# Performance work log

Measured on AMD Instinct MI355X. Metric: run time of the kernel, lower is better.

The kernel has to match this reference:

```python
import jax, jax.numpy as jnp
import numpy as np

O, D, E, K, H, A = 1024, 1024, 16, 4, 2048, 64  # option_dim, obs_dim, num_experts, k, moe_hidden, act_dim
LOSS_COEF = 0.01


def cv_squared(x):
    # torch .var() is unbiased (ddof=1)
    eps = 1e-10
    return jnp.var(x, ddof=1) / (jnp.mean(x) ** 2 + eps)


def setup_inputs() -> dict:
    key = jax.random.key(0)
    ks = jax.random.split(key, 8)
    s = 0.02
    return {
        "obs": jax.random.normal(ks[0], (O, D), jnp.float32),
        # original inits w_gate to zeros (degenerate top-k); use small random for a meaningful baseline
        "w_gate": jax.random.normal(ks[1], (O, D, E), jnp.float32) * s,
        "w1": jax.random.normal(ks[2], (E, D, H), jnp.float32) * s,   # expert MLP layer 1
        "b1": jnp.zeros((E, H), jnp.float32),
        "w2": jax.random.normal(ks[3], (E, H, A), jnp.float32) * s,   # expert MLP layer 2
        "b2": jnp.zeros((E, A), jnp.float32),
        "last_w": jax.random.normal(ks[4], (O, D, A), jnp.float32),   # last_w_layer
        "last_b": jax.random.normal(ks[5], (O, A), jnp.float32),      # last_b_layer
    }


def reference(obs, w_gate, w1, b1, w2, b2, last_w, last_b):
    # ---- noisy_top_k_gating (this version applies no noise) ----
    logits = jnp.einsum('od,ode->oe', obs, w_gate)                    # [O, E]
    top_vals, top_idx = jax.lax.top_k(logits, K + 1)
    topk_gates = jax.nn.softmax(top_vals[:, :K], axis=1)              # softmax over top-k logits
    rows = jnp.arange(O)[:, None]
    gates = jnp.zeros_like(logits).at[rows, top_idx[:, :K]].set(topk_gates)  # scatter -> [O, E]
    importance = gates.sum(axis=1)
    load = (gates > 0).sum(axis=1).astype(jnp.float32)                # faithful to original (sum over dim 1)
    loss = (cv_squared(importance) + cv_squared(load)) * LOSS_COEF
    # ---- dispatch / expert MLPs / combine (dense-over-experts equivalent; zero gates kill non-top-k) ----
    h = jax.nn.relu(jnp.einsum('od,edh->oeh', obs, w1) + b1[None])    # [O, E, H]
    y = jnp.einsum('oe,oeh,eha->oa', gates, h, w2) + gates @ b2       # [O, A]
    # ---- action head ----
    mu = jnp.einsum('od,oda->oa', obs, last_w) + last_b               # [O, A]
    action_probs = jax.nn.softmax(mu, axis=-1)
    z = (action_probs == 0.0).astype(action_probs.dtype) * 1e-08
    log_action_probs = jnp.log(action_probs + z)
    return (action_probs, log_action_probs, y, loss)
```

## Files before the change

### kernel.cpp

```cpp
#include <hip/hip_runtime.h>
#include <hip/hip_bf16.h>
#include <math.h>

#define O_ 1024
#define D_ 1024
#define E_ 16
#define K_ 4
#define H_ 2048
#define A_ 64
#define LOSS_COEF 0.01f

#define FLT_MIN_NORMAL 1.17549435e-38f

using floatx4 = __attribute__((ext_vector_type(4))) float;
using fragb   = __attribute__((ext_vector_type(8))) short;

static __device__ __forceinline__ ushort f2bf(float f) {
    unsigned u = __builtin_bit_cast(unsigned, f);
    u += 0x7fffu + ((u >> 16) & 1u);
    return (ushort)(u >> 16);
}

static __device__ __forceinline__ void gld_lds16(const void* g, void* l) {
    __builtin_amdgcn_global_load_lds(
        (const __attribute__((address_space(1))) void*)g,
        (__attribute__((address_space(3))) void*)l, 16, 0, 0);
}

__global__ __launch_bounds__(256) void gating_kernel(
    const float* __restrict__ obs, const float* __restrict__ w_gate,
    int* __restrict__ topk_idx, float* __restrict__ topk_gate,
    float* __restrict__ imp, float* __restrict__ loadv)
{
    const int o = blockIdx.x;
    const int t = threadIdx.x;
    __shared__ float xs[D_];
    __shared__ float part[64][20];
    __shared__ float logits[E_];

    const float4* xrow = (const float4*)(obs + (size_t)o * D_);
    for (int i = t; i < D_ / 4; i += 256) ((float4*)xs)[i] = xrow[i];
    __syncthreads();

    const int dg = t >> 2, e4 = t & 3;
    const float4* wg = (const float4*)(w_gate + (size_t)o * (D_ * E_));
    float4 acc = make_float4(0.f, 0.f, 0.f, 0.f);
    #pragma unroll 4
    for (int i = 0; i < 16; ++i) {
        int d = dg + (i << 6);
        float4 w = wg[d * 4 + e4];
        float x = xs[d];
        acc.x += x * w.x; acc.y += x * w.y; acc.z += x * w.z; acc.w += x * w.w;
    }
    *(float4*)&part[dg][e4 * 4] = acc;
    __syncthreads();
    if (t < E_) {
        float s = 0.f;
        for (int g = 0; g < 64; ++g) s += part[g][t];
        logits[t] = s;
    }
    __syncthreads();
    if (t == 0) {
        float lv[E_];
        #pragma unroll
        for (int i = 0; i < E_; ++i) lv[i] = logits[i];
        int idx[K_]; float val[K_];
        bool used[E_] = {};
        for (int k = 0; k < K_; ++k) {
            int bi = 0; float bv = -INFINITY;
            for (int i = 0; i < E_; ++i)
                if (!used[i] && lv[i] > bv) { bv = lv[i]; bi = i; }
            used[bi] = true; idx[k] = bi; val[k] = bv;
        }
        float m = val[0];
        float ex[K_]; float s = 0.f;
        for (int k = 0; k < K_; ++k) { ex[k] = expf(val[k] - m); s += ex[k]; }
        float inv = 1.f / s;
        float sumg = 0.f; int ld = 0;
        for (int k = 0; k < K_; ++k) {
            float g = ex[k] * inv;
            topk_idx[o * K_ + k] = idx[k];
            topk_gate[o * K_ + k] = g;
            sumg += g;
            if (g > 0.f) ld++;
        }
        imp[o] = sumg;
        loadv[o] = (float)ld;
    }
}

__global__ void zero_cnt_kernel(int* __restrict__ cnt)
{
    if (threadIdx.x < E_) cnt[threadIdx.x] = 0;
}

__global__ __launch_bounds__(256) void build_dispatch_kernel(
    const int* __restrict__ topk_idx, const float* __restrict__ topk_gate,
    int* __restrict__ cnt, int* __restrict__ rows, float* __restrict__ gatev)
{
    int i = blockIdx.x * 256 + threadIdx.x;
    int e = topk_idx[i];
    int pos = atomicAdd(&cnt[e], 1);
    rows[e * O_ + pos] = i >> 2;
    gatev[e * O_ + pos] = topk_gate[i];
}

__global__ __launch_bounds__(64) void y_init_kernel(
    const int* __restrict__ topk_idx, const float* __restrict__ topk_gate,
    const float* __restrict__ b2, float* __restrict__ y)
{
    int o = blockIdx.x, a = threadIdx.x;
    float acc = 0.f;
    #pragma unroll
    for (int k = 0; k < K_; ++k) {
        int e = topk_idx[o * K_ + k];
        acc += topk_gate[o * K_ + k] * b2[e * A_ + a];
    }
    y[(size_t)o * A_ + a] = acc;
}

__global__ __launch_bounds__(1024) void loss_kernel(
    const float* __restrict__ imp, const float* __restrict__ loadv,
    float* __restrict__ out_loss)
{
    __shared__ float s1[1024], s2[1024];
    __shared__ float mean1, mean2;
    int t = threadIdx.x;
    float a = imp[t], b = loadv[t];
    s1[t] = a; s2[t] = b; __syncthreads();
    for (int s = 512; s > 0; s >>= 1) {
        if (t < s) { s1[t] += s1[t + s]; s2[t] += s2[t + s]; }
        __syncthreads();
    }
    if (t == 0) { mean1 = s1[0] / O_; mean2 = s2[0] / O_; }
    __syncthreads();
    float d1 = a - mean1, d2 = b - mean2;
    s1[t] = d1 * d1; s2[t] = d2 * d2; __syncthreads();
    for (int s = 512; s > 0; s >>= 1) {
        if (t < s) { s1[t] += s1[t + s]; s2[t] += s2[t + s]; }
        __syncthreads();
    }
    if (t == 0) {
        float var1 = s1[0] / (O_ - 1), var2 = s2[0] / (O_ - 1);
        const float eps = 1e-10f;
        out_loss[0] = (var1 / (mean1 * mean1 + eps) + var2 / (mean2 * mean2 + eps)) * LOSS_COEF;
    }
}

__global__ __launch_bounds__(256) void cvt_obs_kernel(
    const float* __restrict__ src, ushort* __restrict__ dst)
{
    int i = blockIdx.x * 256 + threadIdx.x;
    float4 v = ((const float4*)src)[i];
    ushort4 u;
    u.x = f2bf(v.x); u.y = f2bf(v.y); u.z = f2bf(v.z); u.w = f2bf(v.w);
    ((ushort4*)dst)[i] = u;
}

__global__ __launch_bounds__(256) void transpose_bf16_kernel(
    const float* __restrict__ src, ushort* __restrict__ dst, int R, int C)
{
    const int c0 = blockIdx.x * 64, r0 = blockIdx.y * 64, e = blockIdx.z;
    __shared__ ushort tile[64][72];
    const float* s = src + (size_t)e * R * C;
    const int t = threadIdx.x;
    const int rr = t >> 4, cq = t & 15;
    #pragma unroll
    for (int i = 0; i < 4; ++i) {
        int r = rr + i * 16;
        float4 v = *(const float4*)(s + (size_t)(r0 + r) * C + c0 + cq * 4);
        ushort4 u;
        u.x = f2bf(v.x); u.y = f2bf(v.y); u.z = f2bf(v.z); u.w = f2bf(v.w);
        *(ushort4*)&tile[r][cq * 4] = u;
    }
    __syncthreads();
    ushort* dbase = dst + (size_t)e * R * C;
    const int cc = t >> 4, rq = t & 15;
    #pragma unroll
    for (int i = 0; i < 4; ++i) {
        int c = cc + i * 16;
        ushort4 u;
        u.x = tile[rq * 4 + 0][c];
        u.y = tile[rq * 4 + 1][c];
        u.z = tile[rq * 4 + 2][c];
        u.w = tile[rq * 4 + 3][c];
        *(ushort4*)(dbase + (size_t)(c0 + c) * R + r0 + rq * 4) = u;
    }
}

__global__ __launch_bounds__(256, 2) void expert_mfma_kernel(
    const ushort* __restrict__ obs_bf, const ushort* __restrict__ w1T,
    const float* __restrict__ b1, const ushort* __restrict__ w2T,
    const int* __restrict__ cnt, const int* __restrict__ rows,
    const float* __restrict__ gatev, float* __restrict__ y)
{
    const int ht = blockIdx.x, rt = blockIdx.y, e = blockIdx.z;
    const int n = cnt[e];
    if (rt * 128 >= n) return;

    const int t = threadIdx.x, wv = t >> 6, l = t & 63;
    const int lm = l & 15, q = l >> 4;
    const int wr = wv >> 1, wc = wv & 1;

    __shared__ __align__(16) ushort smem[32768];
    __shared__ int   rid_s[128];
    __shared__ float rgate_s[128];
    __shared__ float b1s[128];

    if (t < 128) {
        int gi = rt * 128 + t;
        rid_s[t]   = (gi < n) ? rows[e * O_ + gi]  : -1;
        rgate_s[t] = (gi < n) ? gatev[e * O_ + gi] : 0.f;
    } else {
        b1s[t - 128] = b1[e * H_ + ht * 128 + (t - 128)];
    }
    __syncthreads();

    const int swe = ((l & 7) ^ (l >> 3)) << 3;
    const ushort* asrc[4];
    const ushort* bsrc[4];
    #pragma unroll
    for (int j = 0; j < 4; ++j) {
        int r = (j * 4 + wv) * 8 + (l >> 3);
        int arow = rid_s[r]; if (arow < 0) arow = 0;
        asrc[j] = obs_bf + (size_t)arow * D_ + swe;
        bsrc[j] = w1T + ((size_t)(e * H_ + ht * 128 + r)) * D_ + swe;
    }

    auto stage = [&](int b, int kc) {
        ushort* ab_ = &smem[b * 8192];
        ushort* bb_ = &smem[16384 + b * 8192];
        const int ko = kc * 64;
        #pragma unroll
        for (int j = 0; j < 4; ++j) {
            gld_lds16(asrc[j] + ko, ab_ + (j * 4 + wv) * 512);
            gld_lds16(bsrc[j] + ko, bb_ + (j * 4 + wv) * 512);
        }
    };

    floatx4 acc[4][4] = {};
    int buf = 0;
    stage(0, 0);
    __syncthreads();

    for (int kc = 0; kc < 16; ++kc) {
        if (kc < 15) stage(buf ^ 1, kc + 1);
        const ushort* ab = &smem[buf * 8192];
        const ushort* bb = &smem[16384 + buf * 8192];
        #pragma unroll
        for (int ks = 0; ks < 2; ++ks) {
            const int co = ((ks * 4 + q) ^ (lm & 7)) << 3;
            fragb a[4];
            #pragma unroll
            for (int i = 0; i < 4; ++i)
                a[i] = *(const fragb*)(ab + (wr * 64 + i * 16 + lm) * 64 + co);
            #pragma unroll
            for (int nt = 0; nt < 4; ++nt) {
                fragb b = *(const fragb*)(bb + (wc * 64 + nt * 16 + lm) * 64 + co);
                #pragma unroll
                for (int i = 0; i < 4; ++i)
                    acc[i][nt] = __builtin_amdgcn_mfma_f32_16x16x32_bf16(a[i], b, acc[i][nt], 0, 0, 0);
            }
        }
        __syncthreads();
        buf ^= 1;
    }

    ushort* Hs = smem;
    #pragma unroll
    for (int i = 0; i < 4; ++i) {
        #pragma unroll
        for (int nt = 0; nt < 4; ++nt) {
            const int col = wc * 64 + nt * 16 + lm;
            const float bb = b1s[col];
            #pragma unroll
            for (int r = 0; r < 4; ++r) {
                const int row = wr * 64 + i * 16 + q * 4 + r;
                float h = acc[i][nt][r] + bb;
                h = h > 0.f ? h : 0.f;
                Hs[row * 136 + col] = f2bf(h * rgate_s[row]);
            }
        }
    }
    __syncthreads();

    floatx4 acc2[4][2] = {};
    #pragma unroll
    for (int ks = 0; ks < 4; ++ks) {
        fragb a[4];
        #pragma unroll
        for (int i = 0; i < 4; ++i)
            a[i] = *(const fragb*)(Hs + (wr * 64 + i * 16 + lm) * 136 + ks * 32 + q * 8);
        #pragma unroll
        for (int nt = 0; nt < 2; ++nt) {
            const int acol = wc * 32 + nt * 16 + lm;
            fragb b = *(const fragb*)(w2T + ((size_t)(e * A_ + acol)) * H_ + ht * 128 + ks * 32 + q * 8);
            #pragma unroll
            for (int i = 0; i < 4; ++i)
                acc2[i][nt] = __builtin_amdgcn_mfma_f32_16x16x32_bf16(a[i], b, acc2[i][nt], 0, 0, 0);
        }
    }

    #pragma unroll
    for (int i = 0; i < 4; ++i) {
        #pragma unroll
        for (int r = 0; r < 4; ++r) {
            const int row = wr * 64 + i * 16 + q * 4 + r;
            const int orow = rid_s[row];
            if (orow >= 0) {
                #pragma unroll
                for (int nt = 0; nt < 2; ++nt)
                    atomicAdd(&y[(size_t)orow * A_ + wc * 32 + nt * 16 + lm], acc2[i][nt][r]);
            }
        }
    }
}

__global__ __launch_bounds__(256) void action_head_kernel(
    const float* __restrict__ obs, const float* __restrict__ last_w,
    const float* __restrict__ last_b,
    float* __restrict__ probs, float* __restrict__ logprobs)
{
    const int o = blockIdx.x;
    const int t = threadIdx.x;
    __shared__ float xs[D_];
    __shared__ float red[16][A_];

    const float4* xrow = (const float4*)(obs + (size_t)o * D_);
    for (int i = t; i < D_ / 4; i += 256) ((float4*)xs)[i] = xrow[i];
    __syncthreads();

    const int a4 = t & 15, dg = t >> 4;
    const float* lw = last_w + (size_t)o * (D_ * A_);
    float acc0 = 0.f, acc1 = 0.f, acc2 = 0.f, acc3 = 0.f;
    #pragma unroll 8
    for (int i = 0; i < D_ / 16; ++i) {
        int d = dg + (i << 4);
        float4 w = *(const float4*)(lw + (size_t)d * A_ + a4 * 4);
        float x = xs[d];
        acc0 += x * w.x; acc1 += x * w.y; acc2 += x * w.z; acc3 += x * w.w;
    }
    *(float4*)&red[dg][a4 * 4] = make_float4(acc0, acc1, acc2, acc3);
    __syncthreads();

    if (t < A_) {
        float mu = last_b[(size_t)o * A_ + t];
        #pragma unroll
        for (int g = 0; g < 16; ++g) mu += red[g][t];
        float mx = mu;
        #pragma unroll
        for (int off = 32; off > 0; off >>= 1) mx = fmaxf(mx, __shfl_xor(mx, off, 64));
        float ex = expf(mu - mx);
        if (ex < FLT_MIN_NORMAL) ex = 0.f;
        float s = ex;
        #pragma unroll
        for (int off = 32; off > 0; off >>= 1) s += __shfl_xor(s, off, 64);
        float p = ex / s;
        if (p < FLT_MIN_NORMAL) p = 0.f;
        probs[(size_t)o * A_ + t] = p;
        float z = (p == 0.f) ? 1e-8f : 0.f;
        logprobs[(size_t)o * A_ + t] = logf(p + z);
    }
}

extern "C" void kernel_launch(void* const* d_in, const int* in_sizes, int n_in,
                              void* d_out, int out_size, void* d_ws, size_t ws_size,
                              hipStream_t stream)
{
    const float* obs    = (const float*)d_in[0];
    const float* w_gate = (const float*)d_in[1];
    const float* w1     = (const float*)d_in[2];
    const float* b1     = (const float*)d_in[3];
    const float* w2     = (const float*)d_in[4];
    const float* b2     = (const float*)d_in[5];
    const float* last_w = (const float*)d_in[6];
    const float* last_b = (const float*)d_in[7];

    float* out   = (float*)d_out;
    float* probs = out;
    float* logp  = out + O_ * A_;
    float* yout  = out + 2 * O_ * A_;
    float* loss  = out + 3 * O_ * A_;

    char* ws = (char*)d_ws;
    int*    topk_idx  = (int*)(ws);
    float*  topk_gate = (float*)(ws + (16 << 10));
    float*  imp       = (float*)(ws + (32 << 10));
    float*  loadv     = (float*)(ws + (36 << 10));
    int*    cnt       = (int*)(ws + (40 << 10));
    int*    rows      = (int*)(ws + (41 << 10));
    float*  gatev     = (float*)(ws + (105 << 10));
    ushort* obs_bf    = (ushort*)(ws + (256 << 10));
    ushort* w1T       = (ushort*)(ws + (256 << 10) + (2 << 20));
    ushort* w2T       = (ushort*)(ws + (256 << 10) + (66 << 20));

    hipLaunchKernelGGL(zero_cnt_kernel, dim3(1), dim3(64), 0, stream, cnt);
    hipLaunchKernelGGL(gating_kernel, dim3(O_), dim3(256), 0, stream,
                       obs, w_gate, topk_idx, topk_gate, imp, loadv);
    hipLaunchKernelGGL(build_dispatch_kernel, dim3((O_ * K_) / 256), dim3(256), 0, stream,
                       topk_idx, topk_gate, cnt, rows, gatev);
    hipLaunchKernelGGL(y_init_kernel, dim3(O_), dim3(A_), 0, stream,
                       topk_idx, topk_gate, b2, yout);
    hipLaunchKernelGGL(loss_kernel, dim3(1), dim3(1024), 0, stream, imp, loadv, loss);

    hipLaunchKernelGGL(cvt_obs_kernel, dim3((O_ * D_) / 1024), dim3(256), 0, stream,
                       obs, obs_bf);
    hipLaunchKernelGGL(transpose_bf16_kernel, dim3(H_ / 64, D_ / 64, E_), dim3(256), 0, stream,
                       w1, w1T, D_, H_);
    hipLaunchKernelGGL(transpose_bf16_kernel, dim3(A_ / 64, H_ / 64, E_), dim3(256), 0, stream,
                       w2, w2T, H_, A_);

    hipLaunchKernelGGL(expert_mfma_kernel, dim3(H_ / 128, O_ / 128, E_), dim3(256), 0, stream,
                       obs_bf, w1T, b1, w2T, cnt, rows, gatev, yout);
    hipLaunchKernelGGL(action_head_kernel, dim3(O_), dim3(256), 0, stream,
                       obs, last_w, last_b, probs, logp);
}
```

Measured before the change: 571.5 us.

## Fuse the ten kernel launches into three kernels

Merges zero-count and both weight transposes into one prep kernel. Gating now also does the dispatch build, the bf16 conversion of obs and the y bias init. The expert MFMA, the action head and the loss are merged into a single mega kernel that picks its branch from the block index. The aim is to cut launch overhead and let the independent action-head work overlap with the expert GEMMs. The costs are higher LDS use in the mega kernel, since it declares shared memory for every branch, which may lower occupancy, plus atomic contention in the gating blocks.

```diff
diff --git a/kernel.cpp b/kernel.cpp
--- a/kernel.cpp
+++ b/kernel.cpp
@@ -27,140 +27,26 @@
         (__attribute__((address_space(3))) void*)l, 16, 0, 0);
 }
 
-__global__ __launch_bounds__(256) void gating_kernel(
-    const float* __restrict__ obs, const float* __restrict__ w_gate,
-    int* __restrict__ topk_idx, float* __restrict__ topk_gate,
-    float* __restrict__ imp, float* __restrict__ loadv)
+__global__ __launch_bounds__(256) void prep_kernel(
+    const float* __restrict__ w1, const float* __restrict__ w2,
+    ushort* __restrict__ w1T, ushort* __restrict__ w2T, int* __restrict__ cnt)
 {
-    const int o = blockIdx.x;
-    const int t = threadIdx.x;
-    __shared__ float xs[D_];
-    __shared__ float part[64][20];
-    __shared__ float logits[E_];
-
-    const float4* xrow = (const float4*)(obs + (size_t)o * D_);
-    for (int i = t; i < D_ / 4; i += 256) ((float4*)xs)[i] = xrow[i];
-    __syncthreads();
-
-    const int dg = t >> 2, e4 = t & 3;
-    const float4* wg = (const float4*)(w_gate + (size_t)o * (D_ * E_));
-    float4 acc = make_float4(0.f, 0.f, 0.f, 0.f);
-    #pragma unroll 4
-    for (int i = 0; i < 16; ++i) {
-        int d = dg + (i << 6);
-        float4 w = wg[d * 4 + e4];
-        float x = xs[d];
-        acc.x += x * w.x; acc.y += x * w.y; acc.z += x * w.z; acc.w += x * w.w;
-    }
-    *(float4*)&part[dg][e4 * 4] = acc;
-    __syncthreads();
-    if (t < E_) {
-        float s = 0.f;
-        for (int g = 0; g < 64; ++g) s += part[g][t];
-        logits[t] = s;
-    }
-    __syncthreads();
-    if (t == 0) {
-        float lv[E_];
-        #pragma unroll
-        for (int i = 0; i < E_; ++i) lv[i] = logits[i];
-        int idx[K_]; float val[K_];
-        bool used[E_] = {};
-        for (int k = 0; k < K_; ++k) {
-            int bi = 0; float bv = -INFINITY;
-            for (int i = 0; i < E_; ++i)
-                if (!used[i] && lv[i] > bv) { bv = lv[i]; bi = i; }
-            used[bi] = true; idx[k] = bi; val[k] = bv;
-        }
-        float m = val[0];
-        float ex[K_]; float s = 0.f;
-        for (int k = 0; k < K_; ++k) { ex[k] = expf(val[k] - m); s += ex[k]; }
-        float inv = 1.f / s;
-        float sumg = 0.f; int ld = 0;
-        for (int k = 0; k < K_; ++k) {
-            float g = ex[k] * inv;
-            topk_idx[o * K_ + k] = idx[k];
-            topk_gate[o * K_ + k] = g;
-            sumg += g;
-            if (g > 0.f) ld++;
-        }
-        imp[o] = sumg;
-        loadv[o] = (float)ld;
-    }
-}
-
-__global__ void zero_cnt_kernel(int* __restrict__ cnt)
-{
-    if (threadIdx.x < E_) cnt[threadIdx.x] = 0;
-}
-
-__global__ __launch_bounds__(256) void build_dispatch_kernel(
-    const int* __restrict__ topk_idx, const float* __restrict__ topk_gate,
-    int* __restrict__ cnt, int* __restrict__ rows, float* __restrict__ gatev)
-{
-    int i = blockIdx.x * 256 + threadIdx.x;
-    int e = topk_idx[i];
-    int pos = atomicAdd(&cnt[e], 1);
-    rows[e * O_ + pos] = i >> 2;
-    gatev[e * O_ + pos] = topk_gate[i];
-}
-
-__global__ __launch_bounds__(64) void y_init_kernel(
-    const int* __restrict__ topk_idx, const float* __restrict__ topk_gate,
-    const float* __restrict__ b2, float* __restrict__ y)
-{
-    int o = blockIdx.x, a = threadIdx.x;
-    float acc = 0.f;
-    #pragma unroll
-    for (int k = 0; k < K_; ++k) {
-        int e = topk_idx[o * K_ + k];
-        acc += topk_gate[o * K_ + k] * b2[e * A_ + a];
-    }
-    y[(size_t)o * A_ + a] = acc;
-}
-
-__global__ __launch_bounds__(1024) void loss_kernel(
-    const float* __restrict__ imp, const float* __restrict__ loadv,
-    float* __restrict__ out_loss)
-{
-    __shared__ float s1[1024], s2[1024];
-    __shared__ float mean1, mean2;
-    int t = threadIdx.x;
-    float a = imp[t], b = loadv[t];
-    s1[t] = a; s2[t] = b; __syncthreads();
-    for (int s = 512; s > 0; s >>= 1) {
-        if (t < s) { s1[t] += s1[t + s]; s2[t] += s2[t + s]; }
-        __syncthreads();
-    }
-    if (t == 0) { mean1 = s1[0] / O_; mean2 = s2[0] / O_; }
-    __syncthreads();
-    float d1 = a - mean1, d2 = b - mean2;
-    s1[t] = d1 * d1; s2[t] = d2 * d2; __syncthreads();
-    for (int s = 512; s > 0; s >>= 1) {
-        if (t < s) { s1[t] += s1[t + s]; s2[t] += s2[t + s]; }
-        __syncthreads();
-    }
-    if (t == 0) {
-        float var1 = s1[0] / (O_ - 1), var2 = s2[0] / (O_ - 1);
-        const float eps = 1e-10f;
-        out_loss[0] = (var1 / (mean1 * mean1 + eps) + var2 / (mean2 * mean2 + eps)) * LOSS_COEF;
-    }
-}
-
-__global__ __launch_bounds__(256) void cvt_obs_kernel(
-    const float* __restrict__ src, ushort* __restrict__ dst)
-{
-    int i = blockIdx.x * 256 + threadIdx.x;
-    float4 v = ((const float4*)src)[i];
-    ushort4 u;
-    u.x = f2bf(v.x); u.y = f2bf(v.y); u.z = f2bf(v.z); u.w = f2bf(v.w);
-    ((ushort4*)dst)[i] = u;
-}
-
-__global__ __launch_bounds__(256) void transpose_bf16_kernel(
-    const float* __restrict__ src, ushort* __restrict__ dst, int R, int C)
-{
-    const int c0 = blockIdx.x * 64, r0 = blockIdx.y * 64, e = blockIdx.z;
+    const int bid = blockIdx.x;
+    if (bid == 0) {
+        if (threadIdx.x < E_) cnt[threadIdx.x] = 0;
+        return;
+    }
+    int id = bid - 1;
+    const float* src; ushort* dst; int R, C, c0, r0, e;
+    if (id < 8192) {
+        c0 = (id & 31) * 64; r0 = ((id >> 5) & 15) * 64; e = id >> 9;
+        src = w1; dst = w1T; R = D_; C = H_;
+    } else {
+        id -= 8192;
+        c0 = 0; r0 = (id & 31) * 64; e = id >> 5;
+        src = w2; dst = w2T; R = H_; C = A_;
+    }
+
     __shared__ ushort tile[64][72];
     const float* s = src + (size_t)e * R * C;
     const int t = threadIdx.x;
@@ -188,178 +74,305 @@
     }
 }
 
-__global__ __launch_bounds__(256, 2) void expert_mfma_kernel(
+__global__ __launch_bounds__(256) void gating_kernel(
+    const float* __restrict__ obs, const float* __restrict__ w_gate,
+    const float* __restrict__ b2,
+    int* __restrict__ cnt, int* __restrict__ rows, float* __restrict__ gatev,
+    float* __restrict__ imp, float* __restrict__ loadv,
+    ushort* __restrict__ obs_bf, float* __restrict__ yout)
+{
+    const int o = blockIdx.x;
+    const int t = threadIdx.x;
+    __shared__ float xs[D_];
+    __shared__ float part[64][20];
+    __shared__ float logits[E_];
+    __shared__ int   sidx[K_];
+    __shared__ float sgate[K_];
+
+    const float4* xrow = (const float4*)(obs + (size_t)o * D_);
+    for (int i = t; i < D_ / 4; i += 256) ((float4*)xs)[i] = xrow[i];
+    __syncthreads();
+
+    const int dg = t >> 2, e4 = t & 3;
+    const float4* wg = (const float4*)(w_gate + (size_t)o * (D_ * E_));
+    float4 acc = make_float4(0.f, 0.f, 0.f, 0.f);
+    #pragma unroll 4
+    for (int i = 0; i < 16; ++i) {
+        int d = dg + (i << 6);
+        float4 w = wg[d * 4 + e4];
+        float x = xs[d];
+        acc.x += x * w.x; acc.y += x * w.y; acc.z += x * w.z; acc.w += x * w.w;
+    }
+    *(float4*)&part[dg][e4 * 4] = acc;
+    __syncthreads();
+    if (t < E_) {
+        float s = 0.f;
+        for (int g = 0; g < 64; ++g) s += part[g][t];
+        logits[t] = s;
+    }
+    __syncthreads();
+    if (t == 0) {
+        float lv[E_];
+        #pragma unroll
+        for (int i = 0; i < E_; ++i) lv[i] = logits[i];
+        int idx[K_]; float val[K_];
+        bool used[E_] = {};
+        for (int k = 0; k < K_; ++k) {
+            int bi = 0; float bv = -INFINITY;
+            for (int i = 0; i < E_; ++i)
+                if (!used[i] && lv[i] > bv) { bv = lv[i]; bi = i; }
+            used[bi] = true; idx[k] = bi; val[k] = bv;
+        }
+        float m = val[0];
+        float ex[K_]; float s = 0.f;
+        for (int k = 0; k < K_; ++k) { ex[k] = expf(val[k] - m); s += ex[k]; }
+        float inv = 1.f / s;
+        float sumg = 0.f; int ld = 0;
+        for (int k = 0; k < K_; ++k) {
+            float g = ex[k] * inv;
+            sidx[k] = idx[k]; sgate[k] = g;
+            int pos = atomicAdd(&cnt[idx[k]], 1);
+            rows[idx[k] * O_ + pos]  = o;
+            gatev[idx[k] * O_ + pos] = g;
+            sumg += g;
+            if (g > 0.f) ld++;
+        }
+        imp[o] = sumg;
+        loadv[o] = (float)ld;
+    }
+
+    {
+        float4 v = ((const float4*)xs)[t];
+        ushort4 u;
+        u.x = f2bf(v.x); u.y = f2bf(v.y); u.z = f2bf(v.z); u.w = f2bf(v.w);
+        ((ushort4*)(obs_bf + (size_t)o * D_))[t] = u;
+    }
+    __syncthreads();
+
+    if (t < A_) {
+        float accy = 0.f;
+        #pragma unroll
+        for (int k = 0; k < K_; ++k)
+            accy += sgate[k] * b2[sidx[k] * A_ + t];
+        yout[(size_t)o * A_ + t] = accy;
+    }
+}
+
+__global__ __launch_bounds__(256, 2) void mega_kernel(
     const ushort* __restrict__ obs_bf, const ushort* __restrict__ w1T,
     const float* __restrict__ b1, const ushort* __restrict__ w2T,
     const int* __restrict__ cnt, const int* __restrict__ rows,
-    const float* __restrict__ gatev, float* __restrict__ y)
+    const float* __restrict__ gatev, float* __restrict__ y,
+    const float* __restrict__ obs, const float* __restrict__ last_w,
+    const float* __restrict__ last_b,
+    float* __restrict__ probs, float* __restrict__ logprobs,
+    const float* __restrict__ imp, const float* __restrict__ loadv,
+    float* __restrict__ out_loss)
 {
-    const int ht = blockIdx.x, rt = blockIdx.y, e = blockIdx.z;
-    const int n = cnt[e];
-    if (rt * 128 >= n) return;
-
-    const int t = threadIdx.x, wv = t >> 6, l = t & 63;
-    const int lm = l & 15, q = l >> 4;
-    const int wr = wv >> 1, wc = wv & 1;
+    const int bid = blockIdx.x;
+    const int t = threadIdx.x;
 
     __shared__ __align__(16) ushort smem[32768];
     __shared__ int   rid_s[128];
     __shared__ float rgate_s[128];
     __shared__ float b1s[128];
-
-    if (t < 128) {
-        int gi = rt * 128 + t;
-        rid_s[t]   = (gi < n) ? rows[e * O_ + gi]  : -1;
-        rgate_s[t] = (gi < n) ? gatev[e * O_ + gi] : 0.f;
-    } else {
-        b1s[t - 128] = b1[e * H_ + ht * 128 + (t - 128)];
-    }
-    __syncthreads();
-
-    const int swe = ((l & 7) ^ (l >> 3)) << 3;
-    const ushort* asrc[4];
-    const ushort* bsrc[4];
-    #pragma unroll
-    for (int j = 0; j < 4; ++j) {
-        int r = (j * 4 + wv) * 8 + (l >> 3);
-        int arow = rid_s[r]; if (arow < 0) arow = 0;
-        asrc[j] = obs_bf + (size_t)arow * D_ + swe;
-        bsrc[j] = w1T + ((size_t)(e * H_ + ht * 128 + r)) * D_ + swe;
-    }
-
-    auto stage = [&](int b, int kc) {
-        ushort* ab_ = &smem[b * 8192];
-        ushort* bb_ = &smem[16384 + b * 8192];
-        const int ko = kc * 64;
+    __shared__ float xs[D_];
+    __shared__ float red[16][A_];
+    __shared__ float ls1[256], ls2[256];
+    __shared__ float mean1, mean2;
+
+    if (bid == 0) {
+        float a[4], b[4];
+        float pa = 0.f, pb = 0.f;
         #pragma unroll
         for (int j = 0; j < 4; ++j) {
-            gld_lds16(asrc[j] + ko, ab_ + (j * 4 + wv) * 512);
-            gld_lds16(bsrc[j] + ko, bb_ + (j * 4 + wv) * 512);
-        }
-    };
-
-    floatx4 acc[4][4] = {};
-    int buf = 0;
-    stage(0, 0);
-    __syncthreads();
-
-    for (int kc = 0; kc < 16; ++kc) {
-        if (kc < 15) stage(buf ^ 1, kc + 1);
-        const ushort* ab = &smem[buf * 8192];
-        const ushort* bb = &smem[16384 + buf * 8192];
-        #pragma unroll
-        for (int ks = 0; ks < 2; ++ks) {
-            const int co = ((ks * 4 + q) ^ (lm & 7)) << 3;
-            fragb a[4];
-            #pragma unroll
-            for (int i = 0; i < 4; ++i)
-                a[i] = *(const fragb*)(ab + (wr * 64 + i * 16 + lm) * 64 + co);
-            #pragma unroll
-            for (int nt = 0; nt < 4; ++nt) {
-                fragb b = *(const fragb*)(bb + (wc * 64 + nt * 16 + lm) * 64 + co);
+            a[j] = imp[t + 256 * j]; b[j] = loadv[t + 256 * j];
+            pa += a[j]; pb += b[j];
+        }
+        ls1[t] = pa; ls2[t] = pb; __syncthreads();
+        for (int s = 128; s > 0; s >>= 1) {
+            if (t < s) { ls1[t] += ls1[t + s]; ls2[t] += ls2[t + s]; }
+            __syncthreads();
+        }
+        if (t == 0) { mean1 = ls1[0] / O_; mean2 = ls2[0] / O_; }
+        __syncthreads();
+        pa = 0.f; pb = 0.f;
+        #pragma unroll
+        for (int j = 0; j < 4; ++j) {
+            float d1 = a[j] - mean1, d2 = b[j] - mean2;
+            pa += d1 * d1; pb += d2 * d2;
+        }
+        ls1[t] = pa; ls2[t] = pb; __syncthreads();
+        for (int s = 128; s > 0; s >>= 1) {
+            if (t < s) { ls1[t] += ls1[t + s]; ls2[t] += ls2[t + s]; }
+            __syncthreads();
+        }
+        if (t == 0) {
+            float var1 = ls1[0] / (O_ - 1), var2 = ls2[0] / (O_ - 1);
+            const float eps = 1e-10f;
+            out_loss[0] = (var1 / (mean1 * mean1 + eps) + var2 / (mean2 * mean2 + eps)) * LOSS_COEF;
+        }
+        return;
+    }
+
+    if (bid <= 2048) {
+        const int id = bid - 1;
+        const int ht = id & 15, rt = (id >> 4) & 7, e = id >> 7;
+        const int n = cnt[e];
+        if (rt * 128 >= n) return;
+
+        const int wv = t >> 6, l = t & 63;
+        const int lm = l & 15, q = l >> 4;
+        const int wr = wv >> 1, wc = wv & 1;
+
+        if (t < 128) {
+            int gi = rt * 128 + t;
+            rid_s[t]   = (gi < n) ? rows[e * O_ + gi]  : -1;
+            rgate_s[t] = (gi < n) ? gatev[e * O_ + gi] : 0.f;
+        } else {
+            b1s[t - 128] = b1[e * H_ + ht * 128 + (t - 128)];
+        }
+        __syncthreads();
+
+        const int swe = ((l & 7) ^ (l >> 3)) << 3;
+        const ushort* asrc[4];
+        const ushort* bsrc[4];
+        #pragma unroll
+        for (int j = 0; j < 4; ++j) {
+            int r = (j * 4 + wv) * 8 + (l >> 3);
+            int arow = rid_s[r]; if (arow < 0) arow = 0;
+            asrc[j] = obs_bf + (size_t)arow * D_ + swe;
+            bsrc[j] = w1T + ((size_t)(e * H_ + ht * 128 + r)) * D_ + swe;
+        }
+
+        auto stage = [&](int b, int kc) {
+            ushort* ab_ = &smem[b * 8192];
+            ushort* bb_ = &smem[16384 + b * 8192];
+            const int ko = kc * 64;
+            #pragma unroll
+            for (int j = 0; j < 4; ++j) {
+                gld_lds16(asrc[j] + ko, ab_ + (j * 4 + wv) * 512);
+                gld_lds16(bsrc[j] + ko, bb_ + (j * 4 + wv) * 512);
+            }
+        };
+
+        floatx4 acc[4][4] = {};
+        int buf = 0;
+        stage(0, 0);
+        __syncthreads();
+
+        for (int kc = 0; kc < 16; ++kc) {
+            if (kc < 15) stage(buf ^ 1, kc + 1);
+            const ushort* ab = &smem[buf * 8192];
+            const ushort* bb = &smem[16384 + buf * 8192];
+            #pragma unroll
+            for (int ks = 0; ks < 2; ++ks) {
+                const int co = ((ks * 4 + q) ^ (lm & 7)) << 3;
+                fragb a[4];
                 #pragma unroll
                 for (int i = 0; i < 4; ++i)
-                    acc[i][nt] = __builtin_amdgcn_mfma_f32_16x16x32_bf16(a[i], b, acc[i][nt], 0, 0, 0);
+                    a[i] = *(const fragb*)(ab + (wr * 64 + i * 16 + lm) * 64 + co);
+                #pragma unroll
+                for (int nt = 0; nt < 4; ++nt) {
+                    fragb b = *(const fragb*)(bb + (wc * 64 + nt * 16 + lm) * 64 + co);
+                    #pragma unroll
+                    for (int i = 0; i < 4; ++i)
+                        acc[i][nt] = __builtin_amdgcn_mfma_f32_16x16x32_bf16(a[i], b, acc[i][nt], 0, 0, 0);
+                }
             }
-        }
-        __syncthreads();
-        buf ^= 1;
-    }
-
-    ushort* Hs = smem;
-    #pragma unroll
-    for (int i = 0; i < 4; ++i) {
-        #pragma unroll
-        for (int nt = 0; nt < 4; ++nt) {
-            const int col = wc * 64 + nt * 16 + lm;
-            const float bb = b1s[col];
+            __syncthreads();
+            buf ^= 1;
+        }
+
+        ushort* Hs = smem;
+        #pragma unroll
+        for (int i = 0; i < 4; ++i) {
+            #pragma unroll
+            for (int nt = 0; nt < 4; ++nt) {
+                const int col = wc * 64 + nt * 16 + lm;
+                const float bb = b1s[col];
+                #pragma unroll
+                for (int r = 0; r < 4; ++r) {
+                    const int row = wr * 64 + i * 16 + q * 4 + r;
+                    float h = acc[i][nt][r] + bb;
+                    h = h > 0.f ? h : 0.f;
+                    Hs[row * 136 + col] = f2bf(h * rgate_s[row]);
+                }
+            }
+        }
+        __syncthreads();
+
+        floatx4 acc2[4][2] = {};
+        #pragma unroll
+        for (int ks = 0; ks < 4; ++ks) {
+            fragb a[4];
+            #pragma unroll
+            for (int i = 0; i < 4; ++i)
+                a[i] = *(const fragb*)(Hs + (wr * 64 + i * 16 + lm) * 136 + ks * 32 + q * 8);
+            #pragma unroll
+            for (int nt = 0; nt < 2; ++nt) {
+                const int acol = wc * 32 + nt * 16 + lm;
+                fragb b = *(const fragb*)(w2T + ((size_t)(e * A_ + acol)) * H_ + ht * 128 + ks * 32 + q * 8);
+                #pragma unroll
+                for (int i = 0; i < 4; ++i)
+                    acc2[i][nt] = __builtin_amdgcn_mfma_f32_16x16x32_bf16(a[i], b, acc2[i][nt], 0, 0, 0);
+            }
+        }
+
+        #pragma unroll
+        for (int i = 0; i < 4; ++i) {
             #pragma unroll
             for (int r = 0; r < 4; ++r) {
                 const int row = wr * 64 + i * 16 + q * 4 + r;
-                float h = acc[i][nt][r] + bb;
-                h = h > 0.f ? h : 0.f;
-                Hs[row * 136 + col] = f2bf(h * rgate_s[row]);
+                const int orow = rid_s[row];
+                if (orow >= 0) {
+                    #pragma unroll
+                    for (int nt = 0; nt < 2; ++nt)
+                        atomicAdd(&y[(size_t)orow * A_ + wc * 32 + nt * 16 + lm], acc2[i][nt][r]);
+                }
             }
         }
-    }
-    __syncthreads();
-
-    floatx4 acc2[4][2] = {};
-    #pragma unroll
-    for (int ks = 0; ks < 4; ++ks) {
-        fragb a[4];
-        #pragma unroll
-        for (int i = 0; i < 4; ++i)
-            a[i] = *(const fragb*)(Hs + (wr * 64 + i * 16 + lm) * 136 + ks * 32 + q * 8);
-        #pragma unroll
-        for (int nt = 0; nt < 2; ++nt) {
-            const int acol = wc * 32 + nt * 16 + lm;
-            fragb b = *(const fragb*)(w2T + ((size_t)(e * A_ + acol)) * H_ + ht * 128 + ks * 32 + q * 8);
-            #pragma unroll
-            for (int i = 0; i < 4; ++i)
-                acc2[i][nt] = __builtin_amdgcn_mfma_f32_16x16x32_bf16(a[i], b, acc2[i][nt], 0, 0, 0);
-        }
-    }
-
-    #pragma unroll
-    for (int i = 0; i < 4; ++i) {
-        #pragma unroll
-        for (int r = 0; r < 4; ++r) {
-            const int row = wr * 64 + i * 16 + q * 4 + r;
-            const int orow = rid_s[row];
-            if (orow >= 0) {
-                #pragma unroll
-                for (int nt = 0; nt < 2; ++nt)
-                    atomicAdd(&y[(size_t)orow * A_ + wc * 32 + nt * 16 + lm], acc2[i][nt][r]);
-            }
-        }
-    }
-}
-
-__global__ __launch_bounds__(256) void action_head_kernel(
-    const float* __restrict__ obs, const float* __restrict__ last_w,
-    const float* __restrict__ last_b,
-    float* __restrict__ probs, float* __restrict__ logprobs)
-{
-    const int o = blockIdx.x;
-    const int t = threadIdx.x;
-    __shared__ float xs[D_];
-    __shared__ float red[16][A_];
-
-    const float4* xrow = (const float4*)(obs + (size_t)o * D_);
-    for (int i = t; i < D_ / 4; i += 256) ((float4*)xs)[i] = xrow[i];
-    __syncthreads();
-
-    const int a4 = t & 15, dg = t >> 4;
-    const float* lw = last_w + (size_t)o * (D_ * A_);
-    float acc0 = 0.f, acc1 = 0.f, acc2 = 0.f, acc3 = 0.f;
-    #pragma unroll 8
-    for (int i = 0; i < D_ / 16; ++i) {
-        int d = dg + (i << 4);
-        float4 w = *(const float4*)(lw + (size_t)d * A_ + a4 * 4);
-        float x = xs[d];
-        acc0 += x * w.x; acc1 += x * w.y; acc2 += x * w.z; acc3 += x * w.w;
-    }
-    *(float4*)&red[dg][a4 * 4] = make_float4(acc0, acc1, acc2, acc3);
-    __syncthreads();
-
-    if (t < A_) {
-        float mu = last_b[(size_t)o * A_ + t];
-        #pragma unroll
-        for (int g = 0; g < 16; ++g) mu += red[g][t];
-        float mx = mu;
-        #pragma unroll
-        for (int off = 32; off > 0; off >>= 1) mx = fmaxf(mx, __shfl_xor(mx, off, 64));
-        float ex = expf(mu - mx);
-        if (ex < FLT_MIN_NORMAL) ex = 0.f;
-        float s = ex;
-        #pragma unroll
-        for (int off = 32; off > 0; off >>= 1) s += __shfl_xor(s, off, 64);
-        float p = ex / s;
-        if (p < FLT_MIN_NORMAL) p = 0.f;
-        probs[(size_t)o * A_ + t] = p;
-        float z = (p == 0.f) ? 1e-8f : 0.f;
-        logprobs[(size_t)o * A_ + t] = logf(p + z);
+        return;
+    }
+
+    {
+        const int o = bid - 2049;
+
+        const float4* xrow = (const float4*)(obs + (size_t)o * D_);
+        for (int i = t; i < D_ / 4; i += 256) ((float4*)xs)[i] = xrow[i];
+        __syncthreads();
+
+        const int a4 = t & 15, dg = t >> 4;
+        const float* lw = last_w + (size_t)o * (D_ * A_);
+        float acc0 = 0.f, acc1 = 0.f, acc2 = 0.f, acc3 = 0.f;
+        #pragma unroll 8
+        for (int i = 0; i < D_ / 16; ++i) {
+            int d = dg + (i << 4);
+            float4 w = *(const float4*)(lw + (size_t)d * A_ + a4 * 4);
+            float x = xs[d];
+            acc0 += x * w.x; acc1 += x * w.y; acc2 += x * w.z; acc3 += x * w.w;
+        }
+        *(float4*)&red[dg][a4 * 4] = make_float4(acc0, acc1, acc2, acc3);
+        __syncthreads();
+
+        if (t < A_) {
+            float mu = last_b[(size_t)o * A_ + t];
+            #pragma unroll
+            for (int g = 0; g < 16; ++g) mu += red[g][t];
+            float mx = mu;
+            #pragma unroll
+            for (int off = 32; off > 0; off >>= 1) mx = fmaxf(mx, __shfl_xor(mx, off, 64));
+            float ex = expf(mu - mx);
+            if (ex < FLT_MIN_NORMAL) ex = 0.f;
+            float s = ex;
+            #pragma unroll
+            for (int off = 32; off > 0; off >>= 1) s += __shfl_xor(s, off, 64);
+            float p = ex / s;
+            if (p < FLT_MIN_NORMAL) p = 0.f;
+            probs[(size_t)o * A_ + t] = p;
+            float z = (p == 0.f) ? 1e-8f : 0.f;
+            logprobs[(size_t)o * A_ + t] = logf(p + z);
+        }
     }
 }
 
@@ -383,8 +396,6 @@
     float* loss  = out + 3 * O_ * A_;
 
     char* ws = (char*)d_ws;
-    int*    topk_idx  = (int*)(ws);
-    float*  topk_gate = (float*)(ws + (16 << 10));
     float*  imp       = (float*)(ws + (32 << 10));
     float*  loadv     = (float*)(ws + (36 << 10));
     int*    cnt       = (int*)(ws + (40 << 10));
@@ -394,24 +405,11 @@
     ushort* w1T       = (ushort*)(ws + (256 << 10) + (2 << 20));
     ushort* w2T       = (ushort*)(ws + (256 << 10) + (66 << 20));
 
-    hipLaunchKernelGGL(zero_cnt_kernel, dim3(1), dim3(64), 0, stream, cnt);
+    hipLaunchKernelGGL(prep_kernel, dim3(1 + 8192 + 512), dim3(256), 0, stream,
+                       w1, w2, w1T, w2T, cnt);
     hipLaunchKernelGGL(gating_kernel, dim3(O_), dim3(256), 0, stream,
-                       obs, w_gate, topk_idx, topk_gate, imp, loadv);
-    hipLaunchKernelGGL(build_dispatch_kernel, dim3((O_ * K_) / 256), dim3(256), 0, stream,
-                       topk_idx, topk_gate, cnt, rows, gatev);
-    hipLaunchKernelGGL(y_init_kernel, dim3(O_), dim3(A_), 0, stream,
-                       topk_idx, topk_gate, b2, yout);
-    hipLaunchKernelGGL(loss_kernel, dim3(1), dim3(1024), 0, stream, imp, loadv, loss);
-
-    hipLaunchKernelGGL(cvt_obs_kernel, dim3((O_ * D_) / 1024), dim3(256), 0, stream,
-                       obs, obs_bf);
-    hipLaunchKernelGGL(transpose_bf16_kernel, dim3(H_ / 64, D_ / 64, E_), dim3(256), 0, stream,
-                       w1, w1T, D_, H_);
-    hipLaunchKernelGGL(transpose_bf16_kernel, dim3(A_ / 64, H_ / 64, E_), dim3(256), 0, stream,
-                       w2, w2T, H_, A_);
-
-    hipLaunchKernelGGL(expert_mfma_kernel, dim3(H_ / 128, O_ / 128, E_), dim3(256), 0, stream,
-                       obs_bf, w1T, b1, w2T, cnt, rows, gatev, yout);
-    hipLaunchKernelGGL(action_head_kernel, dim3(O_), dim3(256), 0, stream,
-                       obs, last_w, last_b, probs, logp);
-}
+                       obs, w_gate, b2, cnt, rows, gatev, imp, loadv, obs_bf, yout);
+    hipLaunchKernelGGL(mega_kernel, dim3(1 + 2048 + 1024), dim3(256), 0, stream,
+                       obs_bf, w1T, b1, w2T, cnt, rows, gatev, yout,
+                       obs, last_w, last_b, probs, logp, imp, loadv, loss);
+}
```

New measurement: 569.8 us. About the same (-0.3%).
